# Kernel optimization log

Measured on AMD Instinct MI355X. Metric: run time of the kernel, lower is better.

The kernel has to match this reference:

```python
import jax, jax.numpy as jnp
import numpy as np
import math

CODE_DIMS = [32, 32]
NUM_CODEBOOK = 16
FEAT_DIM = 1024
EPS = 1e-12


def rms_norm(x, eps=EPS):
    var = jnp.mean(x * x, axis=-1, keepdims=True) + eps
    return x * jax.lax.rsqrt(var)


def outer_product(y, code_dims):
    # y: [..., h, sum(code_dims)] -> [..., h, prod(code_dims)]
    splits = list(np.cumsum(code_dims)[:-1])
    mats = jnp.split(y, splits, axis=-1)
    out = mats[0]
    for m in mats[1:]:
        out = out[..., :, None] * m[..., None, :]
        out = out.reshape(*out.shape[:-2], -1)
    return out


def setup_inputs() -> dict:
    key = jax.random.key(0)
    kx, kw = jax.random.split(key)
    x = jax.random.normal(kx, (4, 2048, FEAT_DIM), dtype=jnp.float32)
    std = math.sqrt(2.0 / (FEAT_DIM + sum(CODE_DIMS)))
    weight = jax.random.normal(kw, (NUM_CODEBOOK, FEAT_DIM, sum(CODE_DIMS)), dtype=jnp.float32) * std
    return {"x": x, "weight": weight}


def reference(x, weight):
    h = weight.shape[0]
    # batched per-codebook linear: [..., d] x [h, d, o] -> [..., h, o]
    y = jnp.einsum('...i,hio->...ho', x, weight)
    # chunked outer product per codebook -> [..., h, prod(code_dims)]
    op = outer_product(y, CODE_DIMS)
    out = jnp.mean(op, axis=-2) * math.sqrt(h)
    return rms_norm(out)
```

## Files before the change

kernel.cpp:

```cpp
#include <hip/hip_runtime.h>
#include <hip/hip_bf16.h>

#define KDIM  1024
#define NOUT  1024
#define NTOK  8192
#define NCB   16
#define BM    256
#define BN    128
#define BK    64
#define TILEB 49152
#define NBUF  3

typedef __attribute__((ext_vector_type(8))) short short8;
typedef __attribute__((ext_vector_type(4))) float f32x4;

__device__ static inline unsigned short f2bf(float f) {
    unsigned int u = __float_as_uint(f);
    return (unsigned short)((u + 0x7FFFu + ((u >> 16) & 1u)) >> 16);
}

__device__ static inline float bf2f(unsigned int h) {
    return __uint_as_float(h << 16);
}

__device__ static inline void async_copy16(const void* g, void* l) {
    __builtin_amdgcn_global_load_lds(
        (const __attribute__((address_space(1))) void*)g,
        (__attribute__((address_space(3))) void*)l, 16, 0, 0);
}

__global__ __launch_bounds__(256) void conv_kernel(const float* __restrict__ x,
                                                   const float* __restrict__ W,
                                                   unsigned short* __restrict__ A,
                                                   unsigned short* __restrict__ Bt) {
    int b = blockIdx.x;
    if (b < 4096) {
        int bb = (b & 7) * 512 + (b >> 3);
        int u = bb * 256 + threadIdx.x;
        const float* src = x + (size_t)u * 8;
        float4 v0 = *(const float4*)(src);
        float4 v1 = *(const float4*)(src + 4);
        short8 o;
        o[0] = (short)f2bf(v0.x); o[1] = (short)f2bf(v0.y);
        o[2] = (short)f2bf(v0.z); o[3] = (short)f2bf(v0.w);
        o[4] = (short)f2bf(v1.x); o[5] = (short)f2bf(v1.y);
        o[6] = (short)f2bf(v1.z); o[7] = (short)f2bf(v1.w);
        *(short8*)(A + (size_t)u * 8) = o;
    } else {
        int u = (b - 4096) * 256 + threadIdx.x;
        int n  = u & (NOUT - 1);
        int k0 = (u >> 10) << 3;
        int h = n >> 6, o = n & 63;
        const float* src = W + (size_t)h * KDIM * 64 + o;
        short8 v;
#pragma unroll
        for (int j = 0; j < 8; ++j)
            v[j] = (short)f2bf(src[(size_t)(k0 + j) * 64]);
        *(short8*)(Bt + (size_t)n * KDIM + k0) = v;
    }
}


__device__ __forceinline__ void stage_tile(const unsigned short* __restrict__ A,
                                           const unsigned short* __restrict__ Bt,
                                           char* lbase, int tid, int m0, int n0, int kel) {
    unsigned short* Als = (unsigned short*)lbase;
    unsigned short* Bls = (unsigned short*)(lbase + 32768);
#pragma unroll
    for (int i = 0; i < 4; ++i) {
        int s = i * 512 + tid;
        int row = s >> 3;
        int cs = (s & 7) ^ (row & 7);
        async_copy16(A + (size_t)(m0 + row) * KDIM + kel + cs * 8, Als + s * 8);
    }
#pragma unroll
    for (int i = 0; i < 2; ++i) {
        int s = i * 512 + tid;
        int row = s >> 3;
        int cs = (s & 7) ^ (row & 7);
        async_copy16(Bt + (size_t)(n0 + row) * KDIM + kel + cs * 8, Bls + s * 8);
    }
}

__device__ __forceinline__ void read_frags(const char* lds, int buf, int chunk,
                                           int wm, int wn, int r15, int q,
                                           short8 (&af)[4], short8 (&bf)[4]) {
    const unsigned short* Al = (const unsigned short*)(lds + buf * TILEB);
    const unsigned short* Bl = Al + 16384;
#pragma unroll
    for (int mf = 0; mf < 4; ++mf) {
        int row = wm * 64 + mf * 16 + r15;
        af[mf] = *(const short8*)(Al + row * 64 + (((chunk + q) ^ (row & 7)) << 3));
    }
#pragma unroll
    for (int nf = 0; nf < 4; ++nf) {
        int row = wn * 64 + nf * 16 + r15;
        bf[nf] = *(const short8*)(Bl + row * 64 + (((chunk + q) ^ (row & 7)) << 3));
    }
}

__device__ __forceinline__ void mfma16(short8 (&af)[4], short8 (&bf)[4], f32x4 (&acc)[4][4]) {
    __builtin_amdgcn_s_setprio(1);
#pragma unroll
    for (int mf = 0; mf < 4; ++mf)
#pragma unroll
        for (int nf = 0; nf < 4; ++nf)
            acc[mf][nf] = __builtin_amdgcn_mfma_f32_16x16x32_bf16(af[mf], bf[nf], acc[mf][nf], 0, 0, 0);
    __builtin_amdgcn_s_setprio(0);
}

template <int VM, bool STAGE>
__device__ __forceinline__ void ktile(const unsigned short* __restrict__ A,
                                      const unsigned short* __restrict__ Bt,
                                      char* lds, int tid, int m0, int n0, int kt,
                                      int wm, int wn, int r15, int q,
                                      short8 (&aH0)[4], short8 (&bH0)[4],
                                      short8 (&aH1)[4], short8 (&bH1)[4],
                                      f32x4 (&acc)[4][4]) {
    asm volatile("s_waitcnt vmcnt(%0)" :: "i"(VM) : "memory");
    __builtin_amdgcn_sched_barrier(0);
    __builtin_amdgcn_s_barrier();
    __builtin_amdgcn_sched_barrier(0);
    read_frags(lds, kt % NBUF, 0, wm, wn, r15, q, aH0, bH0);
    read_frags(lds, kt % NBUF, 4, wm, wn, r15, q, aH1, bH1);
    if (STAGE)
        stage_tile(A, Bt, lds + ((kt + 2) % NBUF) * TILEB, tid, m0, n0, (kt + 2) * BK);
    asm volatile("s_waitcnt lgkmcnt(8)" ::: "memory");
    __builtin_amdgcn_sched_barrier(0);
    mfma16(aH0, bH0, acc);
    asm volatile("s_waitcnt lgkmcnt(0)" ::: "memory");
    __builtin_amdgcn_sched_barrier(0);
    mfma16(aH1, bH1, acc);
}

__global__ __launch_bounds__(512, 2) void gemm_kernel(const unsigned short* __restrict__ A,
                                                      const unsigned short* __restrict__ Bt,
                                                      unsigned short* __restrict__ Y) {
    extern __shared__ char lds[];

    const int id  = blockIdx.x;
    const int xcd = id & 7;
    const int j   = id >> 3;
    const int m0  = (xcd * 4 + (j >> 3)) * BM;
    const int n0  = (j & 7) * BN;

    const int tid  = threadIdx.x;
    const int lane = tid & 63;
    const int w    = tid >> 6;
    const int wm   = w >> 1;
    const int wn   = w & 1;
    const int r15  = lane & 15;
    const int q    = lane >> 4;

    f32x4 acc[4][4];
#pragma unroll
    for (int mf = 0; mf < 4; ++mf)
#pragma unroll
        for (int nf = 0; nf < 4; ++nf)
            acc[mf][nf] = (f32x4){0.f, 0.f, 0.f, 0.f};

    short8 aH0[4], bH0[4], aH1[4], bH1[4];

    stage_tile(A, Bt, lds,         tid, m0, n0, 0);
    stage_tile(A, Bt, lds + TILEB, tid, m0, n0, BK);

#pragma unroll 1
    for (int kt = 0; kt < 14; ++kt)
        ktile<6, true>(A, Bt, lds, tid, m0, n0, kt, wm, wn, r15, q, aH0, bH0, aH1, bH1, acc);
    ktile<6, false>(A, Bt, lds, tid, m0, n0, 14, wm, wn, r15, q, aH0, bH0, aH1, bH1, acc);
    ktile<0, false>(A, Bt, lds, tid, m0, n0, 15, wm, wn, r15, q, aH0, bH0, aH1, bH1, acc);

#pragma unroll
    for (int mf = 0; mf < 4; ++mf)
#pragma unroll
        for (int nf = 0; nf < 4; ++nf) {
            int col = n0 + wn * 64 + nf * 16 + r15;
#pragma unroll
            for (int r = 0; r < 4; ++r) {
                int row = m0 + wm * 64 + mf * 16 + q * 4 + r;
                Y[(size_t)row * NOUT + col] = f2bf(acc[mf][nf][r]);
            }
        }
}

__global__ __launch_bounds__(256) void epilogue_kernel(const unsigned short* __restrict__ Y,
                                                       float* __restrict__ out) {
    __shared__ float ylds[1024];
    __shared__ float red[4];

    const int t = (blockIdx.x & 7) * 1024 + (blockIdx.x >> 3);
    const int tid = threadIdx.x;
    const unsigned short* yrow = Y + (size_t)t * NOUT;

    {
        uint2 raw = *(const uint2*)(yrow + tid * 4);
        ylds[tid * 4 + 0] = bf2f(raw.x & 0xffffu);
        ylds[tid * 4 + 1] = bf2f(raw.x >> 16);
        ylds[tid * 4 + 2] = bf2f(raw.y & 0xffffu);
        ylds[tid * 4 + 3] = bf2f(raw.y >> 16);
    }
    __syncthreads();

    const int jj = tid >> 3;
    const int k0 = (tid & 7) * 4;

    float o0 = 0.f, o1 = 0.f, o2 = 0.f, o3 = 0.f;
#pragma unroll
    for (int h = 0; h < NCB; ++h) {
        float a = ylds[h * 64 + jj];
        float4 bb = *(const float4*)&ylds[h * 64 + 32 + k0];
        o0 += a * bb.x; o1 += a * bb.y; o2 += a * bb.z; o3 += a * bb.w;
    }
    o0 *= 0.25f; o1 *= 0.25f; o2 *= 0.25f; o3 *= 0.25f;

    float ss = o0 * o0 + o1 * o1 + o2 * o2 + o3 * o3;
#pragma unroll
    for (int off = 32; off >= 1; off >>= 1)
        ss += __shfl_xor(ss, off, 64);

    const int lane = tid & 63, wv = tid >> 6;
    if (lane == 0) red[wv] = ss;
    __syncthreads();
    float tot = red[0] + red[1] + red[2] + red[3];
    float scale = rsqrtf(tot * (1.0f / 1024.0f) + 1e-12f);

    float4 o;
    o.x = o0 * scale; o.y = o1 * scale; o.z = o2 * scale; o.w = o3 * scale;
    *(float4*)(out + (size_t)t * 1024 + tid * 4) = o;
}

extern "C" void kernel_launch(void* const* d_in, const int* in_sizes, int n_in,
                              void* d_out, int out_size, void* d_ws, size_t ws_size,
                              hipStream_t stream) {
    const float* x   = (const float*)d_in[0];
    const float* wgt = (const float*)d_in[1];
    float* out = (float*)d_out;

    unsigned short* A  = (unsigned short*)d_ws;
    unsigned short* Bt = (unsigned short*)((char*)d_ws + (16u << 20));
    unsigned short* Y  = (unsigned short*)((char*)d_ws + (18u << 20));

    (void)hipFuncSetAttribute((const void*)gemm_kernel,
                              hipFuncAttributeMaxDynamicSharedMemorySize, NBUF * TILEB);

    conv_kernel<<<4096 + 512, 256, 0, stream>>>(x, wgt, A, Bt);
    gemm_kernel<<<(NTOK / BM) * (NOUT / BN), 512, NBUF * TILEB, stream>>>(A, Bt, Y);
    epilogue_kernel<<<NTOK, 256, 0, stream>>>(Y, out);
}
```

Measured before the change: 46.64 us.

## Load A fragments directly from global into registers using blocked layout

The conversion kernel now writes the bf16 activation matrix in a 32x32-blocked layout so that each MFMA A fragment is one contiguous 16-byte global load. The GEMM stops staging A through LDS and instead double-buffers A fragments in registers (aC/aN), prefetching the next k-tile with global_load_dwordx4. Only B is staged in LDS, which shrinks shared memory to 48KB and becomes static. This removes LDS traffic and capacity pressure for A, but adds register pressure and makes the MFMA pipeline depend on global-load latency, with A reuse across the two N-waves now served by cache rather than LDS.

```diff
diff --git a/kernel.cpp b/kernel.cpp
--- a/kernel.cpp
+++ b/kernel.cpp
@@ -8,7 +8,7 @@
 #define BM    256
 #define BN    128
 #define BK    64
-#define TILEB 49152
+#define BBUF  16384
 #define NBUF  3
 
 typedef __attribute__((ext_vector_type(8))) short short8;
@@ -29,15 +29,23 @@
         (__attribute__((address_space(3))) void*)l, 16, 0, 0);
 }
 
+__device__ __forceinline__ short8 gload16(const unsigned short* p) {
+    short8 d;
+    asm volatile("global_load_dwordx4 %0, %1, off" : "=v"(d) : "v"(p) : "memory");
+    return d;
+}
+
 __global__ __launch_bounds__(256) void conv_kernel(const float* __restrict__ x,
                                                    const float* __restrict__ W,
-                                                   unsigned short* __restrict__ A,
+                                                   unsigned short* __restrict__ A2,
                                                    unsigned short* __restrict__ Bt) {
     int b = blockIdx.x;
     if (b < 4096) {
         int bb = (b & 7) * 512 + (b >> 3);
         int u = bb * 256 + threadIdx.x;
-        const float* src = x + (size_t)u * 8;
+        int tok = u >> 7;
+        int k0  = (u & 127) * 8;
+        const float* src = x + (size_t)tok * KDIM + k0;
         float4 v0 = *(const float4*)(src);
         float4 v1 = *(const float4*)(src + 4);
         short8 o;
@@ -45,7 +53,9 @@
         o[2] = (short)f2bf(v0.z); o[3] = (short)f2bf(v0.w);
         o[4] = (short)f2bf(v1.x); o[5] = (short)f2bf(v1.y);
         o[6] = (short)f2bf(v1.z); o[7] = (short)f2bf(v1.w);
-        *(short8*)(A + (size_t)u * 8) = o;
+        size_t dst = (size_t)(tok >> 5) * 32768 + (size_t)(k0 >> 5) * 1024
+                   + (tok & 31) * 32 + (k0 & 31);
+        *(short8*)(A2 + dst) = o;
     } else {
         int u = (b - 4096) * 256 + threadIdx.x;
         int n  = u & (NOUT - 1);
@@ -60,19 +70,9 @@
     }
 }
 
-
-__device__ __forceinline__ void stage_tile(const unsigned short* __restrict__ A,
-                                           const unsigned short* __restrict__ Bt,
-                                           char* lbase, int tid, int m0, int n0, int kel) {
-    unsigned short* Als = (unsigned short*)lbase;
-    unsigned short* Bls = (unsigned short*)(lbase + 32768);
-#pragma unroll
-    for (int i = 0; i < 4; ++i) {
-        int s = i * 512 + tid;
-        int row = s >> 3;
-        int cs = (s & 7) ^ (row & 7);
-        async_copy16(A + (size_t)(m0 + row) * KDIM + kel + cs * 8, Als + s * 8);
-    }
+__device__ __forceinline__ void stage_b(const unsigned short* __restrict__ Bt,
+                                        char* lbase, int tid, int n0, int kel) {
+    unsigned short* Bls = (unsigned short*)lbase;
 #pragma unroll
     for (int i = 0; i < 2; ++i) {
         int s = i * 512 + tid;
@@ -82,23 +82,6 @@
     }
 }
 
-__device__ __forceinline__ void read_frags(const char* lds, int buf, int chunk,
-                                           int wm, int wn, int r15, int q,
-                                           short8 (&af)[4], short8 (&bf)[4]) {
-    const unsigned short* Al = (const unsigned short*)(lds + buf * TILEB);
-    const unsigned short* Bl = Al + 16384;
-#pragma unroll
-    for (int mf = 0; mf < 4; ++mf) {
-        int row = wm * 64 + mf * 16 + r15;
-        af[mf] = *(const short8*)(Al + row * 64 + (((chunk + q) ^ (row & 7)) << 3));
-    }
-#pragma unroll
-    for (int nf = 0; nf < 4; ++nf) {
-        int row = wn * 64 + nf * 16 + r15;
-        bf[nf] = *(const short8*)(Bl + row * 64 + (((chunk + q) ^ (row & 7)) << 3));
-    }
-}
-
 __device__ __forceinline__ void mfma16(short8 (&af)[4], short8 (&bf)[4], f32x4 (&acc)[4][4]) {
     __builtin_amdgcn_s_setprio(1);
 #pragma unroll
@@ -109,40 +92,63 @@
     __builtin_amdgcn_s_setprio(0);
 }
 
-template <int VM, bool STAGE>
-__device__ __forceinline__ void ktile(const unsigned short* __restrict__ A,
+template <int VM, bool IA, bool IB>
+__device__ __forceinline__ void ktile(const unsigned short* const (&ap)[4],
                                       const unsigned short* __restrict__ Bt,
-                                      char* lds, int tid, int m0, int n0, int kt,
-                                      int wm, int wn, int r15, int q,
-                                      short8 (&aH0)[4], short8 (&bH0)[4],
-                                      short8 (&aH1)[4], short8 (&bH1)[4],
+                                      char* lds, int tid, int n0, int kt,
+                                      int wn, int r15, int q,
+                                      short8 (&aC)[4][2], short8 (&aN)[4][2],
                                       f32x4 (&acc)[4][4]) {
     asm volatile("s_waitcnt vmcnt(%0)" :: "i"(VM) : "memory");
     __builtin_amdgcn_sched_barrier(0);
     __builtin_amdgcn_s_barrier();
     __builtin_amdgcn_sched_barrier(0);
-    read_frags(lds, kt % NBUF, 0, wm, wn, r15, q, aH0, bH0);
-    read_frags(lds, kt % NBUF, 4, wm, wn, r15, q, aH1, bH1);
-    if (STAGE)
-        stage_tile(A, Bt, lds + ((kt + 2) % NBUF) * TILEB, tid, m0, n0, (kt + 2) * BK);
-    asm volatile("s_waitcnt lgkmcnt(8)" ::: "memory");
-    __builtin_amdgcn_sched_barrier(0);
-    mfma16(aH0, bH0, acc);
+
+    const unsigned short* Bl = (const unsigned short*)(lds + (kt % NBUF) * BBUF);
+    short8 bf0[4], bf1[4];
+#pragma unroll
+    for (int nf = 0; nf < 4; ++nf) {
+        int row = wn * 64 + nf * 16 + r15;
+        bf0[nf] = *(const short8*)(Bl + row * 64 + ((q ^ (row & 7)) << 3));
+    }
+#pragma unroll
+    for (int nf = 0; nf < 4; ++nf) {
+        int row = wn * 64 + nf * 16 + r15;
+        bf1[nf] = *(const short8*)(Bl + row * 64 + (((4 + q) ^ (row & 7)) << 3));
+    }
+    __builtin_amdgcn_sched_barrier(0);
+    if (IA) {
+#pragma unroll
+        for (int mf = 0; mf < 4; ++mf)
+#pragma unroll
+            for (int h = 0; h < 2; ++h)
+                aN[mf][h] = gload16(ap[mf] + (2 * (kt + 1) + h) * 1024);
+    }
+    __builtin_amdgcn_sched_barrier(0);
+    if (IB)
+        stage_b(Bt, lds + ((kt + 2) % NBUF) * BBUF, tid, n0, (kt + 2) * BK);
+
+    asm volatile("s_waitcnt lgkmcnt(4)" ::: "memory");
+    __builtin_amdgcn_sched_barrier(0);
+    short8 a0[4] = {aC[0][0], aC[1][0], aC[2][0], aC[3][0]};
+    mfma16(a0, bf0, acc);
     asm volatile("s_waitcnt lgkmcnt(0)" ::: "memory");
     __builtin_amdgcn_sched_barrier(0);
-    mfma16(aH1, bH1, acc);
-}
-
-__global__ __launch_bounds__(512, 2) void gemm_kernel(const unsigned short* __restrict__ A,
+    short8 a1[4] = {aC[0][1], aC[1][1], aC[2][1], aC[3][1]};
+    mfma16(a1, bf1, acc);
+}
+
+__global__ __launch_bounds__(512, 2) void gemm_kernel(const unsigned short* __restrict__ A2,
                                                       const unsigned short* __restrict__ Bt,
                                                       unsigned short* __restrict__ Y) {
-    extern __shared__ char lds[];
+    __shared__ char lds[NBUF * BBUF];
 
     const int id  = blockIdx.x;
     const int xcd = id & 7;
     const int j   = id >> 3;
     const int m0  = (xcd * 4 + (j >> 3)) * BM;
     const int n0  = (j & 7) * BN;
+    const int Gb  = m0 >> 5;
 
     const int tid  = threadIdx.x;
     const int lane = tid & 63;
@@ -152,6 +158,12 @@
     const int r15  = lane & 15;
     const int q    = lane >> 4;
 
+    const unsigned short* ap[4];
+#pragma unroll
+    for (int mf = 0; mf < 4; ++mf)
+        ap[mf] = A2 + (size_t)(Gb + 2 * wm + (mf >> 1)) * 32768
+               + ((mf & 1) * 16 + r15) * 32 + q * 8;
+
     f32x4 acc[4][4];
 #pragma unroll
     for (int mf = 0; mf < 4; ++mf)
@@ -159,16 +171,24 @@
         for (int nf = 0; nf < 4; ++nf)
             acc[mf][nf] = (f32x4){0.f, 0.f, 0.f, 0.f};
 
-    short8 aH0[4], bH0[4], aH1[4], bH1[4];
-
-    stage_tile(A, Bt, lds,         tid, m0, n0, 0);
-    stage_tile(A, Bt, lds + TILEB, tid, m0, n0, BK);
+    short8 aC[4][2], aN[4][2];
+
+#pragma unroll
+    for (int mf = 0; mf < 4; ++mf)
+#pragma unroll
+        for (int h = 0; h < 2; ++h)
+            aC[mf][h] = gload16(ap[mf] + h * 1024);
+    __builtin_amdgcn_sched_barrier(0);
+    stage_b(Bt, lds,        tid, n0, 0);
+    stage_b(Bt, lds + BBUF, tid, n0, BK);
 
 #pragma unroll 1
-    for (int kt = 0; kt < 14; ++kt)
-        ktile<6, true>(A, Bt, lds, tid, m0, n0, kt, wm, wn, r15, q, aH0, bH0, aH1, bH1, acc);
-    ktile<6, false>(A, Bt, lds, tid, m0, n0, 14, wm, wn, r15, q, aH0, bH0, aH1, bH1, acc);
-    ktile<0, false>(A, Bt, lds, tid, m0, n0, 15, wm, wn, r15, q, aH0, bH0, aH1, bH1, acc);
+    for (int t2 = 0; t2 < 7; ++t2) {
+        ktile<2, true, true>(ap, Bt, lds, tid, n0, 2 * t2,     wn, r15, q, aC, aN, acc);
+        ktile<2, true, true>(ap, Bt, lds, tid, n0, 2 * t2 + 1, wn, r15, q, aN, aC, acc);
+    }
+    ktile<2, true,  false>(ap, Bt, lds, tid, n0, 14, wn, r15, q, aC, aN, acc);
+    ktile<0, false, false>(ap, Bt, lds, tid, n0, 15, wn, r15, q, aN, aC, acc);
 
 #pragma unroll
     for (int mf = 0; mf < 4; ++mf)
@@ -236,14 +256,11 @@
     const float* wgt = (const float*)d_in[1];
     float* out = (float*)d_out;
 
-    unsigned short* A  = (unsigned short*)d_ws;
+    unsigned short* A2 = (unsigned short*)d_ws;
     unsigned short* Bt = (unsigned short*)((char*)d_ws + (16u << 20));
     unsigned short* Y  = (unsigned short*)((char*)d_ws + (18u << 20));
 
-    (void)hipFuncSetAttribute((const void*)gemm_kernel,
-                              hipFuncAttributeMaxDynamicSharedMemorySize, NBUF * TILEB);
-
-    conv_kernel<<<4096 + 512, 256, 0, stream>>>(x, wgt, A, Bt);
-    gemm_kernel<<<(NTOK / BM) * (NOUT / BN), 512, NBUF * TILEB, stream>>>(A, Bt, Y);
+    conv_kernel<<<4096 + 512, 256, 0, stream>>>(x, wgt, A2, Bt);
+    gemm_kernel<<<(NTOK / BM) * (NOUT / BN), 512, 0, stream>>>(A2, Bt, Y);
     epilogue_kernel<<<NTOK, 256, 0, stream>>>(Y, out);
 }
```

Result: slower. 53.00 us (+13.6%).

## Split k-tile into two half-phases with interleaved staging and barriers

Applied to the files above, without the earlier changes.

Restructures each k-tile iteration into two phases. Each phase reads half the fragments, issues half of the next tile's async global-to-LDS copies, synchronizes with a workgroup barrier, and runs its MFMAs. This halves the fragment registers (one aF/bF set instead of two) and spreads global loads across the MFMA work, in a ping-pong style schedule. It adds several extra s_barrier calls per k-tile, and the MFMAs can no longer overlap with the second fragment read, so added synchronization stalls are a risk.

```diff
diff --git a/kernel.cpp b/kernel.cpp
--- a/kernel.cpp
+++ b/kernel.cpp
@@ -61,21 +61,21 @@
 }
 
 
-__device__ __forceinline__ void stage_tile(const unsigned short* __restrict__ A,
-                                           const unsigned short* __restrict__ Bt,
-                                           char* lbase, int tid, int m0, int n0, int kel) {
+__device__ __forceinline__ void stage_slice(const unsigned short* __restrict__ A,
+                                            const unsigned short* __restrict__ Bt,
+                                            char* lbase, int tid, int m0, int n0,
+                                            int kel, int half) {
     unsigned short* Als = (unsigned short*)lbase;
     unsigned short* Bls = (unsigned short*)(lbase + 32768);
 #pragma unroll
-    for (int i = 0; i < 4; ++i) {
-        int s = i * 512 + tid;
+    for (int i = 0; i < 2; ++i) {
+        int s = (half * 2 + i) * 512 + tid;
         int row = s >> 3;
         int cs = (s & 7) ^ (row & 7);
         async_copy16(A + (size_t)(m0 + row) * KDIM + kel + cs * 8, Als + s * 8);
     }
-#pragma unroll
-    for (int i = 0; i < 2; ++i) {
-        int s = i * 512 + tid;
+    {
+        int s = half * 512 + tid;
         int row = s >> 3;
         int cs = (s & 7) ^ (row & 7);
         async_copy16(Bt + (size_t)(n0 + row) * KDIM + kel + cs * 8, Bls + s * 8);
@@ -114,23 +114,36 @@
                                       const unsigned short* __restrict__ Bt,
                                       char* lds, int tid, int m0, int n0, int kt,
                                       int wm, int wn, int r15, int q,
-                                      short8 (&aH0)[4], short8 (&bH0)[4],
-                                      short8 (&aH1)[4], short8 (&bH1)[4],
+                                      short8 (&aF)[4], short8 (&bF)[4],
                                       f32x4 (&acc)[4][4]) {
+    char* nbuf = lds + ((kt + 2) % NBUF) * TILEB;
+    const int nk = (kt + 2) * BK;
+
     asm volatile("s_waitcnt vmcnt(%0)" :: "i"(VM) : "memory");
     __builtin_amdgcn_sched_barrier(0);
     __builtin_amdgcn_s_barrier();
     __builtin_amdgcn_sched_barrier(0);
-    read_frags(lds, kt % NBUF, 0, wm, wn, r15, q, aH0, bH0);
-    read_frags(lds, kt % NBUF, 4, wm, wn, r15, q, aH1, bH1);
+    read_frags(lds, kt % NBUF, 0, wm, wn, r15, q, aF, bF);
     if (STAGE)
-        stage_tile(A, Bt, lds + ((kt + 2) % NBUF) * TILEB, tid, m0, n0, (kt + 2) * BK);
-    asm volatile("s_waitcnt lgkmcnt(8)" ::: "memory");
-    __builtin_amdgcn_sched_barrier(0);
-    mfma16(aH0, bH0, acc);
+        stage_slice(A, Bt, nbuf, tid, m0, n0, nk, 0);
+    __builtin_amdgcn_sched_barrier(0);
+    __builtin_amdgcn_s_barrier();
     asm volatile("s_waitcnt lgkmcnt(0)" ::: "memory");
     __builtin_amdgcn_sched_barrier(0);
-    mfma16(aH1, bH1, acc);
+    mfma16(aF, bF, acc);
+    __builtin_amdgcn_sched_barrier(0);
+    __builtin_amdgcn_s_barrier();
+
+    __builtin_amdgcn_sched_barrier(0);
+    read_frags(lds, kt % NBUF, 4, wm, wn, r15, q, aF, bF);
+    if (STAGE)
+        stage_slice(A, Bt, nbuf, tid, m0, n0, nk, 1);
+    __builtin_amdgcn_sched_barrier(0);
+    __builtin_amdgcn_s_barrier();
+    asm volatile("s_waitcnt lgkmcnt(0)" ::: "memory");
+    __builtin_amdgcn_sched_barrier(0);
+    mfma16(aF, bF, acc);
+    __builtin_amdgcn_sched_barrier(0);
 }
 
 __global__ __launch_bounds__(512, 2) void gemm_kernel(const unsigned short* __restrict__ A,
@@ -159,16 +172,18 @@
         for (int nf = 0; nf < 4; ++nf)
             acc[mf][nf] = (f32x4){0.f, 0.f, 0.f, 0.f};
 
-    short8 aH0[4], bH0[4], aH1[4], bH1[4];
-
-    stage_tile(A, Bt, lds,         tid, m0, n0, 0);
-    stage_tile(A, Bt, lds + TILEB, tid, m0, n0, BK);
+    short8 aF[4], bF[4];
+
+    stage_slice(A, Bt, lds,         tid, m0, n0, 0,  0);
+    stage_slice(A, Bt, lds,         tid, m0, n0, 0,  1);
+    stage_slice(A, Bt, lds + TILEB, tid, m0, n0, BK, 0);
+    stage_slice(A, Bt, lds + TILEB, tid, m0, n0, BK, 1);
 
 #pragma unroll 1
     for (int kt = 0; kt < 14; ++kt)
-        ktile<6, true>(A, Bt, lds, tid, m0, n0, kt, wm, wn, r15, q, aH0, bH0, aH1, bH1, acc);
-    ktile<6, false>(A, Bt, lds, tid, m0, n0, 14, wm, wn, r15, q, aH0, bH0, aH1, bH1, acc);
-    ktile<0, false>(A, Bt, lds, tid, m0, n0, 15, wm, wn, r15, q, aH0, bH0, aH1, bH1, acc);
+        ktile<6, true>(A, Bt, lds, tid, m0, n0, kt, wm, wn, r15, q, aF, bF, acc);
+    ktile<6, false>(A, Bt, lds, tid, m0, n0, 14, wm, wn, r15, q, aF, bF, acc);
+    ktile<0, false>(A, Bt, lds, tid, m0, n0, 15, wm, wn, r15, q, aF, bF, acc);
 
 #pragma unroll
     for (int mf = 0; mf < 4; ++mf)
```

Result: no change. 47.35 us (+1.5%).
